# Performance work log

Hardware: AMD Instinct MI355X
Metric: run time of the kernel (lower is better)

Reference implementation:

```python
import jax, jax.numpy as jnp
import numpy as np

D_STATE = 16
LOW_RANK = 6


def _scan_fwd(t):
    # 'interwave' scan: (B, stream, signal, C, H, W) -> (stream, B, C, H*W*signal)
    st, B, C = t.shape[1], t.shape[0], t.shape[3]
    t = jnp.transpose(t, (1, 0, 3, 4, 5, 2))  # stream,B,C,H,W,signal
    return t.reshape(st, B, C, -1)


def _scan_bwd(t, sg, H, W):
    # inverse 'interwave': (stream, B, C, H*W*sg) -> (B, stream, sg, C, H, W)
    st, B, C, _ = t.shape
    t = t.reshape(st, B, C, H, W, sg)
    return jnp.transpose(t, (1, 0, 5, 2, 3, 4))


def _layernorm(t, w, b):
    # LayerNorm over last (channel) axis, eps=1e-5 (torch default)
    mu = t.mean(-1, keepdims=True)
    var = t.var(-1, keepdims=True)
    return (t - mu) * jax.lax.rsqrt(var + 1e-5) * w + b


def reference(x, x_proj_weight, dt_projs_weight, dt_projs_bias, A_logs, Ds, norm_weight, norm_bias):
    B, S, C, H, W = x.shape
    stream = S + 1
    G = 4 * stream            # scan_direction * stream groups
    N = D_STATE
    R = LOW_RANK
    L = S * H * W             # unistream_length
    i = jnp.arange(S - 1)
    j = jnp.arange(S)

    # ---- CommDiffSS2DScan (cross-scan) ----
    x_comm_0 = _scan_fwd(x[:, None])                                  # (1,B,C,L)
    x_comm_1 = _scan_fwd(jnp.swapaxes(x, -1, -2)[:, None])
    x_dif = x[:, :, None] - x[:, None, :]                             # (B,S,S,C,H,W)
    x_dif = x_dif.at[:, i, i].set(x_dif[:, i, S - 1])
    x_dif = x_dif.at[:, :, S - 1].set(x)
    x_diff_0 = _scan_fwd(x_dif)                                       # (S,B,C,L)
    x_diff_1 = _scan_fwd(jnp.swapaxes(x_dif, -1, -2))
    xs0 = jnp.concatenate([x_diff_0, x_comm_0], 0)                    # (stream,B,C,L)
    xs1 = jnp.concatenate([x_diff_1, x_comm_1], 0)
    xs = jnp.stack([xs0, xs1, xs0[..., ::-1], xs1[..., ::-1]], 0)     # (4,stream,B,C,L)
    xs = jnp.transpose(xs, (2, 0, 1, 3, 4))                           # (B,4,stream,C,L)

    # ---- input-dependent projections ----
    x_dbl = jnp.einsum('bkscl,kspc->bkspl', xs, x_proj_weight)        # (B,4,stream,R+2N,L)
    dts, Bs, Cs = jnp.split(x_dbl, [R, R + N], axis=3)
    dts = jnp.einsum('bksrl,kscr->bkscl', dts, dt_projs_weight)       # (B,4,stream,C,L)

    u = xs.reshape(B, G, C, L)
    delta = jax.nn.softplus(dts.reshape(B, G, C, L) + dt_projs_bias.reshape(G, C)[None, :, :, None])
    A = -jnp.exp(A_logs).reshape(G, C, N)
    Bm = Bs.reshape(B, G, N, L)
    Cm = Cs.reshape(B, G, N, L)

    # ---- selective scan along L ----
    def step(h, inp):
        u_, d_, b_, c_ = inp                                          # (B,G,C),(B,G,C),(B,G,N),(B,G,N)
        h = h * jnp.exp(d_[..., None] * A) + (d_ * u_)[..., None] * b_[:, :, None, :]
        return h, jnp.einsum('bgcn,bgn->bgc', h, c_)

    h0 = jnp.zeros((B, G, C, N), x.dtype)
    _, ys = jax.lax.scan(step, h0, (jnp.moveaxis(u, -1, 0), jnp.moveaxis(delta, -1, 0),
                                    jnp.moveaxis(Bm, -1, 0), jnp.moveaxis(Cm, -1, 0)))
    ys = jnp.moveaxis(ys, 0, -1) + Ds.reshape(G, C)[None, :, :, None] * u  # (B,G,C,L)

    # ---- CommDiffSS2DMerge (cross-merge) ----
    ys = jnp.transpose(ys.reshape(B, 4, stream, C, L), (1, 2, 0, 3, 4))   # (4,stream,B,C,L)
    ys = ys[:2] + ys[2:, ..., ::-1]                                       # (2,stream,B,C,L)
    yd = _scan_bwd(ys[0, :S], S, H, W) + jnp.swapaxes(_scan_bwd(ys[1, :S], S, W, H), -1, -2)
    y = yd[:, :, S - 1]
    yd = yd.at[:, i, S - 1].set(yd[:, i, i])
    yd = yd.at[:, j, j].set(0.0)
    y_dif_extend = yd.sum(2)
    y_com = (_scan_bwd(ys[0, S:], S, H, W) + jnp.swapaxes(_scan_bwd(ys[1, S:], S, W, H), -1, -2)).reshape(B, S, C, H, W)

    tocl = lambda t: jnp.transpose(t, (0, 1, 3, 4, 2))  # channels-last for out_norm
    return (_layernorm(tocl(y), norm_weight, norm_bias),
            _layernorm(tocl(y_com), norm_weight, norm_bias),
            _layernorm(tocl(y_dif_extend), norm_weight, norm_bias))


def setup_inputs() -> dict:
    key = jax.random.key(0)
    ks = jax.random.split(key, 6)
    B, S, C, H, W = 4, 2, 96, 32, 32
    stream = S + 1
    G = 4 * stream
    N, R = D_STATE, LOW_RANK
    P = N + N + R
    return {
        'x': jax.random.normal(ks[0], (B, S, C, H, W), jnp.float32),
        'x_proj_weight': jax.random.normal(ks[1], (4, stream, P, C), jnp.float32) * 0.1,
        'dt_projs_weight': jax.random.normal(ks[2], (4, stream, C, R), jnp.float32) * 0.1,
        'dt_projs_bias': jax.random.uniform(ks[3], (G * C,), jnp.float32) * 0.1,
        'A_logs': jax.random.uniform(ks[4], (G * C, N), jnp.float32),
        'Ds': jax.random.normal(ks[5], (G * C,), jnp.float32) * 0.1,
        'norm_weight': jnp.ones((C,), jnp.float32),
        'norm_bias': jnp.zeros((C,), jnp.float32),
    }
```

## Files before the change

### kernel.cpp

```cpp
#include <hip/hip_runtime.h>
#include <math.h>

typedef float f4 __attribute__((ext_vector_type(4)));
typedef float f2 __attribute__((ext_vector_type(2)));

#define L_LEN 2048
#define C_DIM 96
#define N_DIM 16
#define R_DIM 6
#define G_DIM 12
#define B_DIM 4
#define NCHUNK 64
#define CLEN 32
#define BGC (B_DIM * G_DIM * C_DIM)

#define SZ_DTS (B_DIM * G_DIM * L_LEN * R_DIM)
#define SZ_BC (B_DIM * G_DIM * N_DIM * L_LEN)
#define SZ_U6 (B_DIM * 6 * C_DIM * L_LEN)
#define SZ_Y (B_DIM * G_DIM * C_DIM * L_LEN)
#define SZ_H (BGC * NCHUNK * N_DIM)
#define SZ_X (B_DIM * 2 * C_DIM * 1024)
#define SZ_WPAD (G_DIM * 40 * C_DIM)

__device__ __forceinline__ float fexp2(float x) { return __builtin_amdgcn_exp2f(x); }

__global__ __launch_bounds__(256) void k0_xT(
    const float* __restrict__ x, float* __restrict__ xT)
{
    __shared__ float t[32][33];
    int img = blockIdx.x;
    const float* src = x + (size_t)img * 1024;
    float* dst = xT + (size_t)img * 1024;
    int tx = threadIdx.x & 31, ty = threadIdx.x >> 5;
#pragma unroll
    for (int r = 0; r < 32; r += 8) t[ty + r][tx] = src[(ty + r) * 32 + tx];
    __syncthreads();
#pragma unroll
    for (int r = 0; r < 32; r += 8) dst[(ty + r) * 32 + tx] = t[tx][ty + r];
}

__global__ __launch_bounds__(256) void k0b_padw(
    const float* __restrict__ xpw, float* __restrict__ wpad)
{
    int i = blockIdx.x * 256 + (int)threadIdx.x;
    if (i >= G_DIM * 40 * C_DIM) return;
    int g = i / (40 * C_DIM);
    int rem = i - g * 40 * C_DIM;
    int p = rem / C_DIM, c = rem - (rem / C_DIM) * C_DIM;
    wpad[i] = (p < 38) ? xpw[((size_t)g * 38 + p) * C_DIM + c] : 0.f;
}

__global__ __launch_bounds__(256) void k1_proj(
    const float* __restrict__ x, const float* __restrict__ xT,
    const float* __restrict__ wpad,
    float* __restrict__ dtsT, float* __restrict__ Bsw,
    float* __restrict__ Csw, float* __restrict__ u6T)
{
    __shared__ float Vsh[C_DIM * 68];
    __shared__ float Psh[40][68];

    int blk = blockIdx.x;
    int ltile = blk & 31;
    int bks = blk >> 5;
    int s = bks % 3;
    int k = (bks / 3) & 1;
    int b = bks / 6;
    int g = k * 3 + s;
    int gh = g + 6;
    int l0 = ltile * 64;
    int l0h = (31 - ltile) * 64;
    int bg = b * G_DIM + g;
    int bgh = b * G_DIM + gh;
    int tid = (int)threadIdx.x;

    const float* xb = (k ? xT : x) + (size_t)b * 2 * C_DIM * 1024;

#pragma unroll
    for (int j = 0; j < 6; ++j) {
        int e = tid + j * 256;
        int c = e >> 4;
        int llq = (e & 15) * 4;
        int pp = (l0 + llq) >> 1;
        f2 x0 = *(const f2*)(xb + (size_t)c * 1024 + pp);
        f2 x1 = *(const f2*)(xb + (size_t)(C_DIM + c) * 1024 + pp);
        f4 v;
        if (s == 2)      { v[0] = x0.x; v[1] = x1.x; v[2] = x0.y; v[3] = x1.y; }
        else if (s == 1) { v[0] = x1.x - x0.x; v[1] = x1.x; v[2] = x1.y - x0.y; v[3] = x1.y; }
        else             { v[0] = x0.x - x1.x; v[1] = x0.x; v[2] = x0.y - x1.y; v[3] = x0.y; }
        *(f4*)(Vsh + c * 68 + llq) = v;
    }
    __syncthreads();

    {
        size_t ub = ((size_t)(b * 6 + g) * L_LEN + l0) * C_DIM;
#pragma unroll
        for (int j = 0; j < 6; ++j) {
            int e = tid + j * 256;
            int lidx = e / 24;
            int c4 = (e - lidx * 24) * 4;
            f4 v = { Vsh[(c4 + 0) * 68 + lidx], Vsh[(c4 + 1) * 68 + lidx],
                     Vsh[(c4 + 2) * 68 + lidx], Vsh[(c4 + 3) * 68 + lidx] };
            *(f4*)(u6T + ub + (size_t)lidx * C_DIM + c4) = v;
        }
    }

    int ll = tid & 63;
    int P0 = __builtin_amdgcn_readfirstlane((tid >> 6) * 10);
    const float* wp = wpad + (size_t)g * 3840 + (size_t)P0 * C_DIM;
    const float* wph = wpad + (size_t)gh * 3840 + (size_t)P0 * C_DIM;

    float acc[10], acch[10];
#pragma unroll
    for (int p = 0; p < 10; ++p) { acc[p] = 0.f; acch[p] = 0.f; }

    for (int cb = 0; cb < C_DIM; cb += 8) {
        float vc[8], vch[8];
#pragma unroll
        for (int i = 0; i < 8; ++i) {
            vc[i] = Vsh[(cb + i) * 68 + ll];
            vch[i] = Vsh[(cb + i) * 68 + 63 - ll];
        }
#pragma unroll
        for (int p = 0; p < 10; ++p) {
#pragma unroll
            for (int q = 0; q < 2; ++q) {
                f4 w = *(const f4*)(wp + p * C_DIM + cb + q * 4);
                f4 wh = *(const f4*)(wph + p * C_DIM + cb + q * 4);
#pragma unroll
                for (int i = 0; i < 4; ++i) {
                    acc[p] = fmaf(w[i], vc[q * 4 + i], acc[p]);
                    acch[p] = fmaf(wh[i], vch[q * 4 + i], acch[p]);
                }
            }
        }
    }

#pragma unroll
    for (int gg = 0; gg < 2; ++gg) {
        __syncthreads();
#pragma unroll
        for (int p = 0; p < 10; ++p) Psh[P0 + p][ll] = gg ? acch[p] : acc[p];
        __syncthreads();
        int lb = gg ? l0h : l0;
        int bgx = gg ? bgh : bg;
        int q = tid & 3, lx = tid >> 2;
        f4 bv = { Psh[6 + q * 4 + 0][lx], Psh[6 + q * 4 + 1][lx],
                  Psh[6 + q * 4 + 2][lx], Psh[6 + q * 4 + 3][lx] };
        *(f4*)(Bsw + ((size_t)bgx * L_LEN + lb + lx) * N_DIM + q * 4) = bv;
        f4 cv = { Psh[22 + q * 4 + 0][lx], Psh[22 + q * 4 + 1][lx],
                  Psh[22 + q * 4 + 2][lx], Psh[22 + q * 4 + 3][lx] };
        *(f4*)(Csw + ((size_t)bgx * L_LEN + lb + lx) * N_DIM + q * 4) = cv;
        for (int e = tid; e < 64 * R_DIM; e += 256) {
            int lx2 = e / 6, r = e - (e / 6) * 6;
            dtsT[((size_t)bgx * L_LEN + lb + lx2) * R_DIM + r] = Psh[r][lx2];
        }
    }
}

__device__ __forceinline__ float softplus_f(float x)
{
    float sp = __logf(1.f + __expf(x));
    return (x > 60.f) ? x : sp;
}

__global__ __launch_bounds__(192) void k2_scanA(
    const float* __restrict__ dtsT, const float* __restrict__ Bsw,
    const float* __restrict__ u6T, const float* __restrict__ A_logs,
    const float* __restrict__ dtw, const float* __restrict__ dtb,
    float* __restrict__ hend, float* __restrict__ prodE)
{
    __shared__ f4 Bsh[256];
    __shared__ float Dsh[384];
    int blk = blockIdx.x;
    int chgrp = blk & 31;
    int bg = blk >> 5;
    int g = bg % G_DIM;
    int b = bg / G_DIM;
    int tid = (int)threadIdx.x;

    const f4* Bg = (const f4*)(Bsw + ((size_t)bg * L_LEN + chgrp * 64) * N_DIM);
    for (int i = tid; i < 256; i += 192) Bsh[i] = Bg[i];
    const float* Dg = dtsT + ((size_t)bg * L_LEN + chgrp * 64) * R_DIM;
    for (int i = tid; i < 384; i += 192) Dsh[i] = Dg[i];
    __syncthreads();

    int chl = tid / 96;
    int c = tid % 96;
    int ch = chgrp * 2 + chl;
    int bgc = bg * C_DIM + c;
    const bool rev = (g >= 6);
    int gu = rev ? (g - 6) : g;

    float a2[N_DIM];
    {
        const f4* Ap = (const f4*)(A_logs + ((size_t)g * C_DIM + c) * N_DIM);
        f4 Av[4] = { Ap[0], Ap[1], Ap[2], Ap[3] };
#pragma unroll
        for (int n = 0; n < N_DIM; ++n)
            a2[n] = -__expf(Av[n >> 2][n & 3]) * 1.44269504f;
    }
    float wdr[R_DIM];
    {
        const float* wdp = dtw + ((size_t)g * C_DIM + c) * R_DIM;
#pragma unroll
        for (int r = 0; r < R_DIM; ++r) wdr[r] = wdp[r];
    }
    float bias = dtb[g * C_DIM + c];

    const int LOFF = ch * CLEN;
    const float* up;
    int ustep;
    if (rev) { up = u6T + ((size_t)(b * 6 + gu) * L_LEN + (2047 - LOFF)) * C_DIM + c; ustep = -C_DIM; }
    else     { up = u6T + ((size_t)(b * 6 + gu) * L_LEN + LOFF) * C_DIM + c; ustep = C_DIM; }

    float h[N_DIM];
#pragma unroll
    for (int n = 0; n < N_DIM; ++n) h[n] = 0.f;
    float S = 0.f;

    float ubuf[4];
#pragma unroll
    for (int j = 0; j < 4; ++j) ubuf[j] = up[j * ustep];

    for (int jj = 0; jj < CLEN; jj += 4) {
        int nx = (jj + 4 < CLEN) ? jj + 4 : jj;
        float un[4];
#pragma unroll
        for (int j = 0; j < 4; ++j) un[j] = up[(nx + j) * ustep];
#pragma unroll
        for (int j = 0; j < 4; ++j) {
            int li = chl * CLEN + jj + j;
            float dt_ = bias;
#pragma unroll
            for (int r = 0; r < R_DIM; ++r) dt_ = fmaf(Dsh[li * R_DIM + r], wdr[r], dt_);
            float d = softplus_f(dt_);
            S += d;
            float du = d * ubuf[j];
            const f4* Bl = Bsh + (size_t)li * 4;
            f4 Bv[4] = { Bl[0], Bl[1], Bl[2], Bl[3] };
#pragma unroll
            for (int n = 0; n < N_DIM; ++n) {
                float e = fexp2(d * a2[n]);
                h[n] = fmaf(h[n], e, du * Bv[n >> 2][n & 3]);
            }
        }
#pragma unroll
        for (int j = 0; j < 4; ++j) ubuf[j] = un[j];
    }
    float* hp = hend + ((size_t)bgc * NCHUNK + ch) * N_DIM;
    float* pp = prodE + ((size_t)bgc * NCHUNK + ch) * N_DIM;
#pragma unroll
    for (int q = 0; q < 4; ++q) {
        f4 hv = { h[q * 4], h[q * 4 + 1], h[q * 4 + 2], h[q * 4 + 3] };
        f4 pv = { fexp2(a2[q * 4] * S), fexp2(a2[q * 4 + 1] * S),
                  fexp2(a2[q * 4 + 2] * S), fexp2(a2[q * 4 + 3] * S) };
        *(f4*)(hp + q * 4) = hv;
        *(f4*)(pp + q * 4) = pv;
    }
}

__global__ __launch_bounds__(256) void k2_fix(
    const float* __restrict__ hend, float* prodE_hstart)
{
    int t = blockIdx.x * 256 + (int)threadIdx.x;
    int n = t & 15;
    int bgc = t >> 4;
    float h = 0.f;
    for (int ch = 0; ch < NCHUNK; ++ch) {
        size_t idx = ((size_t)bgc * NCHUNK + ch) * N_DIM + n;
        float Pv = prodE_hstart[idx];
        float he = hend[idx];
        prodE_hstart[idx] = h;
        h = fmaf(h, Pv, he);
    }
}

__global__ __launch_bounds__(192) void k2_scanC(
    const float* __restrict__ dtsT, const float* __restrict__ Bsw,
    const float* __restrict__ Csw, const float* __restrict__ u6T,
    const float* __restrict__ A_logs, const float* __restrict__ Ds,
    const float* __restrict__ dtw, const float* __restrict__ dtb,
    const float* __restrict__ hstart, float* __restrict__ yssT)
{
    __shared__ f4 Bsh[256];
    __shared__ f4 Csh[256];
    __shared__ float Dsh[384];
    int blk = blockIdx.x;
    int chgrp = blk & 31;
    int bg = blk >> 5;
    int g = bg % G_DIM;
    int b = bg / G_DIM;
    int tid = (int)threadIdx.x;

    const f4* Bg = (const f4*)(Bsw + ((size_t)bg * L_LEN + chgrp * 64) * N_DIM);
    const f4* Cg = (const f4*)(Csw + ((size_t)bg * L_LEN + chgrp * 64) * N_DIM);
    for (int i = tid; i < 256; i += 192) { Bsh[i] = Bg[i]; Csh[i] = Cg[i]; }
    const float* Dg = dtsT + ((size_t)bg * L_LEN + chgrp * 64) * R_DIM;
    for (int i = tid; i < 384; i += 192) Dsh[i] = Dg[i];
    __syncthreads();

    int chl = tid / 96;
    int c = tid % 96;
    int ch = chgrp * 2 + chl;
    int bgc = bg * C_DIM + c;
    const bool rev = (g >= 6);
    int gu = rev ? (g - 6) : g;

    float a2[N_DIM];
    {
        const f4* Ap = (const f4*)(A_logs + ((size_t)g * C_DIM + c) * N_DIM);
        f4 Av[4] = { Ap[0], Ap[1], Ap[2], Ap[3] };
#pragma unroll
        for (int n = 0; n < N_DIM; ++n)
            a2[n] = -__expf(Av[n >> 2][n & 3]) * 1.44269504f;
    }
    float wdr[R_DIM];
    {
        const float* wdp = dtw + ((size_t)g * C_DIM + c) * R_DIM;
#pragma unroll
        for (int r = 0; r < R_DIM; ++r) wdr[r] = wdp[r];
    }
    float bias = dtb[g * C_DIM + c];
    float dsc = Ds[g * C_DIM + c];

    const int LOFF = ch * CLEN;
    const float* up;
    int ustep;
    if (rev) { up = u6T + ((size_t)(b * 6 + gu) * L_LEN + (2047 - LOFF)) * C_DIM + c; ustep = -C_DIM; }
    else     { up = u6T + ((size_t)(b * 6 + gu) * L_LEN + LOFF) * C_DIM + c; ustep = C_DIM; }
    float* yp = yssT + ((size_t)bg * L_LEN + LOFF) * C_DIM + c;

    float h[N_DIM];
    {
        const f4* Hp = (const f4*)(hstart + ((size_t)bgc * NCHUNK + ch) * N_DIM);
        f4 Hv[4] = { Hp[0], Hp[1], Hp[2], Hp[3] };
#pragma unroll
        for (int n = 0; n < N_DIM; ++n) h[n] = Hv[n >> 2][n & 3];
    }

    float ubuf[4];
#pragma unroll
    for (int j = 0; j < 4; ++j) ubuf[j] = up[j * ustep];

    for (int jj = 0; jj < CLEN; jj += 4) {
        int nx = (jj + 4 < CLEN) ? jj + 4 : jj;
        float un[4];
#pragma unroll
        for (int j = 0; j < 4; ++j) un[j] = up[(nx + j) * ustep];
#pragma unroll
        for (int j = 0; j < 4; ++j) {
            int li = chl * CLEN + jj + j;
            float dt_ = bias;
#pragma unroll
            for (int r = 0; r < R_DIM; ++r) dt_ = fmaf(Dsh[li * R_DIM + r], wdr[r], dt_);
            float d = softplus_f(dt_);
            float uu = ubuf[j];
            float du = d * uu;
            const f4* Bl = Bsh + (size_t)li * 4;
            const f4* Cl = Csh + (size_t)li * 4;
            f4 Bv[4] = { Bl[0], Bl[1], Bl[2], Bl[3] };
            f4 Cv[4] = { Cl[0], Cl[1], Cl[2], Cl[3] };
            float y0 = dsc * uu, y1 = 0.f, y2 = 0.f, y3 = 0.f;
#pragma unroll
            for (int q = 0; q < 4; ++q) {
                float e0 = fexp2(d * a2[q * 4 + 0]);
                float e1 = fexp2(d * a2[q * 4 + 1]);
                float e2 = fexp2(d * a2[q * 4 + 2]);
                float e3 = fexp2(d * a2[q * 4 + 3]);
                h[q * 4 + 0] = fmaf(h[q * 4 + 0], e0, du * Bv[q][0]);
                h[q * 4 + 1] = fmaf(h[q * 4 + 1], e1, du * Bv[q][1]);
                h[q * 4 + 2] = fmaf(h[q * 4 + 2], e2, du * Bv[q][2]);
                h[q * 4 + 3] = fmaf(h[q * 4 + 3], e3, du * Bv[q][3]);
                y0 = fmaf(h[q * 4 + 0], Cv[q][0], y0);
                y1 = fmaf(h[q * 4 + 1], Cv[q][1], y1);
                y2 = fmaf(h[q * 4 + 2], Cv[q][2], y2);
                y3 = fmaf(h[q * 4 + 3], Cv[q][3], y3);
            }
            yp[(jj + j) * C_DIM] = (y0 + y1) + (y2 + y3);
        }
#pragma unroll
        for (int j = 0; j < 4; ++j) ubuf[j] = un[j];
    }
}

__global__ __launch_bounds__(256) void k3_out(
    const float* __restrict__ yssT, const float* __restrict__ nw,
    const float* __restrict__ nb, float* __restrict__ out)
{
    __shared__ float tA[32][97];
    __shared__ float tB[32][97];
    __shared__ float ps[4][8][32];
    __shared__ float stat[4][32];

    int blk = blockIdx.x;
    int h = blk & 31;
    int bs = blk >> 5;
    int so = bs & 1;
    int b = bs >> 1;
    int tid = (int)threadIdx.x;

    auto Y = [&](int g) { return yssT + (size_t)(b * 12 + g) * L_LEN * C_DIM; };
    const float* Y0 = Y(so);
    const float* Y0r = Y(6 + so);
    const float* Y1 = Y(3 + so);
    const float* Y1r = Y(9 + so);

#pragma unroll 2
    for (int it = 0; it < 24; ++it) {
        int idx = tid + it * 256;
        int c = idx % 96, rest = idx / 96;
        int w = rest >> 1, par = rest & 1;
        int a0 = h * 64 + rest;
        int a1 = w * 64 + 2 * h + par;
        float v = Y0[(size_t)a0 * C_DIM + c] + Y0r[(size_t)(2047 - a0) * C_DIM + c]
                + Y1[(size_t)a1 * C_DIM + c] + Y1r[(size_t)(2047 - a1) * C_DIM + c];
        if (par) tA[w][c] = v; else tB[w][c] = v;
    }
    __syncthreads();

    int w = tid & 31, cg = tid >> 5;
    float sA = 0, qA = 0, sB = 0, qB = 0;
#pragma unroll
    for (int j = 0; j < 12; ++j) {
        float yv = tA[w][cg * 12 + j], dv = tB[w][cg * 12 + j];
        sA += yv; qA += yv * yv; sB += dv; qB += dv * dv;
    }
    ps[0][cg][w] = sA; ps[1][cg][w] = qA; ps[2][cg][w] = sB; ps[3][cg][w] = qB;
    __syncthreads();
    if (tid < 32) {
        int ww = tid;
        float t0 = 0, t1 = 0, t2 = 0, t3 = 0;
#pragma unroll
        for (int q = 0; q < 8; ++q) {
            t0 += ps[0][q][ww]; t1 += ps[1][q][ww];
            t2 += ps[2][q][ww]; t3 += ps[3][q][ww];
        }
        float muA = t0 * (1.f / 96.f), eqA = t1 * (1.f / 96.f);
        float muB = t2 * (1.f / 96.f), eqB = t3 * (1.f / 96.f);
        stat[0][ww] = muA; stat[1][ww] = rsqrtf(eqA - muA * muA + 1e-5f);
        stat[2][ww] = muB; stat[3][ww] = rsqrtf(eqB - muB * muB + 1e-5f);
    }
    __syncthreads();
    size_t obase = (size_t)blk * 3072;
    for (int e = tid; e < 3072; e += 256) {
        int ww = e / 96, c = e % 96;
        float wc = nw[c], bc = nb[c];
        out[obase + e] = (tA[ww][c] - stat[0][ww]) * stat[1][ww] * wc + bc;
        out[2 * 786432 + obase + e] = (tB[ww][c] - stat[2][ww]) * stat[3][ww] * wc + bc;
    }
    __syncthreads();

    const float* Y2 = Y(2);
    const float* Y2r = Y(8);
    const float* Y3 = Y(5);
    const float* Y3r = Y(11);
#pragma unroll 2
    for (int it = 0; it < 12; ++it) {
        int idx = tid + it * 256;
        int c = idx % 96, w2 = idx / 96;
        int a0 = h * 64 + 2 * w2 + so;
        int a1 = w2 * 64 + 2 * h + so;
        float v = Y2[(size_t)a0 * C_DIM + c] + Y2r[(size_t)(2047 - a0) * C_DIM + c]
                + Y3[(size_t)a1 * C_DIM + c] + Y3r[(size_t)(2047 - a1) * C_DIM + c];
        tA[w2][c] = v;
    }
    __syncthreads();
    float sC = 0, qC = 0;
#pragma unroll
    for (int j = 0; j < 12; ++j) {
        float v = tA[w][cg * 12 + j];
        sC += v; qC += v * v;
    }
    ps[0][cg][w] = sC; ps[1][cg][w] = qC;
    __syncthreads();
    if (tid < 32) {
        int ww = tid;
        float t0 = 0, t1 = 0;
#pragma unroll
        for (int q = 0; q < 8; ++q) { t0 += ps[0][q][ww]; t1 += ps[1][q][ww]; }
        float mu = t0 * (1.f / 96.f), eq = t1 * (1.f / 96.f);
        stat[0][ww] = mu; stat[1][ww] = rsqrtf(eq - mu * mu + 1e-5f);
    }
    __syncthreads();
    for (int e = tid; e < 3072; e += 256) {
        int ww = e / 96, c = e % 96;
        out[786432 + obase + e] = (tA[ww][c] - stat[0][ww]) * stat[1][ww] * nw[c] + nb[c];
    }
}

extern "C" void kernel_launch(void* const* d_in, const int* in_sizes, int n_in,
                              void* d_out, int out_size, void* d_ws, size_t ws_size,
                              hipStream_t stream)
{
    const float* x = (const float*)d_in[0];
    const float* xpw = (const float*)d_in[1];
    const float* dtw = (const float*)d_in[2];
    const float* dtb = (const float*)d_in[3];
    const float* A_logs = (const float*)d_in[4];
    const float* Ds = (const float*)d_in[5];
    const float* nw = (const float*)d_in[6];
    const float* nb = (const float*)d_in[7];
    float* out = (float*)d_out;

    float* ws = (float*)d_ws;
    float* dtsT = ws;
    float* Bsw = dtsT + SZ_DTS;
    float* Csw = Bsw + SZ_BC;
    float* u6T = Csw + SZ_BC;
    float* yssT = u6T + SZ_U6;
    float* hend = yssT + SZ_Y;
    float* prodE = hend + SZ_H;
    float* xT = prodE + SZ_H;
    float* wpad = xT + SZ_X;

    k0_xT<<<dim3(768), dim3(256), 0, stream>>>(x, xT);
    k0b_padw<<<dim3(180), dim3(256), 0, stream>>>(xpw, wpad);
    k1_proj<<<dim3(24 * 32), dim3(256), 0, stream>>>(x, xT, wpad, dtsT, Bsw, Csw, u6T);
    k2_scanA<<<dim3(48 * 32), dim3(192), 0, stream>>>(dtsT, Bsw, u6T, A_logs, dtw, dtb, hend, prodE);
    k2_fix<<<dim3(288), dim3(256), 0, stream>>>(hend, prodE);
    k2_scanC<<<dim3(48 * 32), dim3(192), 0, stream>>>(dtsT, Bsw, Csw, u6T, A_logs, Ds, dtw, dtb, prodE, yssT);
    k3_out<<<dim3(256), dim3(256), 0, stream>>>(yssT, nw, nb, out);
}
```

Before: 154.3 us.

## Scan kernels read B/C/dt directly as wave-uniform loads in single-wave blocks

The two scan kernels drop the shared-memory staging of B, C and dt rows and the block-wide barrier, and instead read them straight from global memory with addresses that are uniform across the wave, so they can become scalar loads. Blocks shrink from 192 threads to one 64-lane wave covering one chunk and half of the channels. The dt projection buffer is padded to 8 entries per position for aligned access. This wastes 32 of every 128 lanes on channel padding and relies on the scalar cache for reuse.

```diff
diff --git a/kernel.cpp b/kernel.cpp
--- a/kernel.cpp
+++ b/kernel.cpp
@@ -14,7 +14,7 @@
 #define CLEN 32
 #define BGC (B_DIM * G_DIM * C_DIM)
 
-#define SZ_DTS (B_DIM * G_DIM * L_LEN * R_DIM)
+#define SZ_DTS8 (B_DIM * G_DIM * L_LEN * 8)
 #define SZ_BC (B_DIM * G_DIM * N_DIM * L_LEN)
 #define SZ_U6 (B_DIM * 6 * C_DIM * L_LEN)
 #define SZ_Y (B_DIM * G_DIM * C_DIM * L_LEN)
@@ -53,7 +53,7 @@
 __global__ __launch_bounds__(256) void k1_proj(
     const float* __restrict__ x, const float* __restrict__ xT,
     const float* __restrict__ wpad,
-    float* __restrict__ dtsT, float* __restrict__ Bsw,
+    float* __restrict__ dts8, float* __restrict__ Bsw,
     float* __restrict__ Csw, float* __restrict__ u6T)
 {
     __shared__ float Vsh[C_DIM * 68];
@@ -150,9 +150,9 @@
         f4 cv = { Psh[22 + q * 4 + 0][lx], Psh[22 + q * 4 + 1][lx],
                   Psh[22 + q * 4 + 2][lx], Psh[22 + q * 4 + 3][lx] };
         *(f4*)(Csw + ((size_t)bgx * L_LEN + lb + lx) * N_DIM + q * 4) = cv;
-        for (int e = tid; e < 64 * R_DIM; e += 256) {
-            int lx2 = e / 6, r = e - (e / 6) * 6;
-            dtsT[((size_t)bgx * L_LEN + lb + lx2) * R_DIM + r] = Psh[r][lx2];
+        for (int e = tid; e < 64 * 8; e += 256) {
+            int lx2 = e >> 3, r = e & 7;
+            dts8[((size_t)bgx * L_LEN + lb + lx2) * 8 + r] = (r < 6) ? Psh[r][lx2] : 0.f;
         }
     }
 }
@@ -163,37 +163,32 @@
     return (x > 60.f) ? x : sp;
 }
 
-__global__ __launch_bounds__(192) void k2_scanA(
-    const float* __restrict__ dtsT, const float* __restrict__ Bsw,
+__global__ __launch_bounds__(64) void k2_scanA(
+    const float* __restrict__ dts8, const float* __restrict__ Bsw,
     const float* __restrict__ u6T, const float* __restrict__ A_logs,
     const float* __restrict__ dtw, const float* __restrict__ dtb,
     float* __restrict__ hend, float* __restrict__ prodE)
 {
-    __shared__ f4 Bsh[256];
-    __shared__ float Dsh[384];
+    int lane = (int)threadIdx.x;
     int blk = blockIdx.x;
-    int chgrp = blk & 31;
-    int bg = blk >> 5;
+    int ctile = blk & 1;
+    int ch = (blk >> 1) & 63;
+    int bg = blk >> 7;
     int g = bg % G_DIM;
     int b = bg / G_DIM;
-    int tid = (int)threadIdx.x;
-
-    const f4* Bg = (const f4*)(Bsw + ((size_t)bg * L_LEN + chgrp * 64) * N_DIM);
-    for (int i = tid; i < 256; i += 192) Bsh[i] = Bg[i];
-    const float* Dg = dtsT + ((size_t)bg * L_LEN + chgrp * 64) * R_DIM;
-    for (int i = tid; i < 384; i += 192) Dsh[i] = Dg[i];
-    __syncthreads();
-
-    int chl = tid / 96;
-    int c = tid % 96;
-    int ch = chgrp * 2 + chl;
-    int bgc = bg * C_DIM + c;
+    int c = ctile * 64 + lane;
+    const bool act = (c < C_DIM);
+    int cc = act ? c : (C_DIM - 1);
     const bool rev = (g >= 6);
     int gu = rev ? (g - 6) : g;
+    const int LOFF = ch * CLEN;
+
+    const float* Brow = Bsw + ((size_t)bg * L_LEN + LOFF) * N_DIM;
+    const float* Drow = dts8 + ((size_t)bg * L_LEN + LOFF) * 8;
 
     float a2[N_DIM];
     {
-        const f4* Ap = (const f4*)(A_logs + ((size_t)g * C_DIM + c) * N_DIM);
+        const f4* Ap = (const f4*)(A_logs + ((size_t)g * C_DIM + cc) * N_DIM);
         f4 Av[4] = { Ap[0], Ap[1], Ap[2], Ap[3] };
 #pragma unroll
         for (int n = 0; n < N_DIM; ++n)
@@ -201,61 +196,48 @@
     }
     float wdr[R_DIM];
     {
-        const float* wdp = dtw + ((size_t)g * C_DIM + c) * R_DIM;
+        const float* wdp = dtw + ((size_t)g * C_DIM + cc) * R_DIM;
 #pragma unroll
         for (int r = 0; r < R_DIM; ++r) wdr[r] = wdp[r];
     }
-    float bias = dtb[g * C_DIM + c];
-
-    const int LOFF = ch * CLEN;
+    float bias = dtb[g * C_DIM + cc];
+
     const float* up;
-    int ustep;
-    if (rev) { up = u6T + ((size_t)(b * 6 + gu) * L_LEN + (2047 - LOFF)) * C_DIM + c; ustep = -C_DIM; }
-    else     { up = u6T + ((size_t)(b * 6 + gu) * L_LEN + LOFF) * C_DIM + c; ustep = C_DIM; }
+    int us;
+    if (rev) { up = u6T + ((size_t)(b * 6 + gu) * L_LEN + (2047 - LOFF)) * C_DIM + cc; us = -C_DIM; }
+    else     { up = u6T + ((size_t)(b * 6 + gu) * L_LEN + LOFF) * C_DIM + cc; us = C_DIM; }
 
     float h[N_DIM];
 #pragma unroll
     for (int n = 0; n < N_DIM; ++n) h[n] = 0.f;
     float S = 0.f;
 
-    float ubuf[4];
-#pragma unroll
-    for (int j = 0; j < 4; ++j) ubuf[j] = up[j * ustep];
-
-    for (int jj = 0; jj < CLEN; jj += 4) {
-        int nx = (jj + 4 < CLEN) ? jj + 4 : jj;
-        float un[4];
-#pragma unroll
-        for (int j = 0; j < 4; ++j) un[j] = up[(nx + j) * ustep];
-#pragma unroll
-        for (int j = 0; j < 4; ++j) {
-            int li = chl * CLEN + jj + j;
-            float dt_ = bias;
-#pragma unroll
-            for (int r = 0; r < R_DIM; ++r) dt_ = fmaf(Dsh[li * R_DIM + r], wdr[r], dt_);
-            float d = softplus_f(dt_);
-            S += d;
-            float du = d * ubuf[j];
-            const f4* Bl = Bsh + (size_t)li * 4;
-            f4 Bv[4] = { Bl[0], Bl[1], Bl[2], Bl[3] };
-#pragma unroll
-            for (int n = 0; n < N_DIM; ++n) {
-                float e = fexp2(d * a2[n]);
-                h[n] = fmaf(h[n], e, du * Bv[n >> 2][n & 3]);
-            }
-        }
-#pragma unroll
-        for (int j = 0; j < 4; ++j) ubuf[j] = un[j];
-    }
-    float* hp = hend + ((size_t)bgc * NCHUNK + ch) * N_DIM;
-    float* pp = prodE + ((size_t)bgc * NCHUNK + ch) * N_DIM;
-#pragma unroll
-    for (int q = 0; q < 4; ++q) {
-        f4 hv = { h[q * 4], h[q * 4 + 1], h[q * 4 + 2], h[q * 4 + 3] };
-        f4 pv = { fexp2(a2[q * 4] * S), fexp2(a2[q * 4 + 1] * S),
-                  fexp2(a2[q * 4 + 2] * S), fexp2(a2[q * 4 + 3] * S) };
-        *(f4*)(hp + q * 4) = hv;
-        *(f4*)(pp + q * 4) = pv;
+#pragma unroll 2
+    for (int j = 0; j < CLEN; ++j) {
+        float dt_ = bias;
+#pragma unroll
+        for (int r = 0; r < R_DIM; ++r) dt_ = fmaf(Drow[j * 8 + r], wdr[r], dt_);
+        float d = softplus_f(dt_);
+        S += d;
+        float du = d * up[j * us];
+#pragma unroll
+        for (int n = 0; n < N_DIM; ++n) {
+            float e = fexp2(d * a2[n]);
+            h[n] = fmaf(h[n], e, du * Brow[j * N_DIM + n]);
+        }
+    }
+    if (act) {
+        int bgc = bg * C_DIM + c;
+        float* hp = hend + ((size_t)bgc * NCHUNK + ch) * N_DIM;
+        float* pp = prodE + ((size_t)bgc * NCHUNK + ch) * N_DIM;
+#pragma unroll
+        for (int q = 0; q < 4; ++q) {
+            f4 hv = { h[q * 4], h[q * 4 + 1], h[q * 4 + 2], h[q * 4 + 3] };
+            f4 pv = { fexp2(a2[q * 4] * S), fexp2(a2[q * 4 + 1] * S),
+                      fexp2(a2[q * 4 + 2] * S), fexp2(a2[q * 4 + 3] * S) };
+            *(f4*)(hp + q * 4) = hv;
+            *(f4*)(pp + q * 4) = pv;
+        }
     }
 }
 
@@ -275,40 +257,34 @@
     }
 }
 
-__global__ __launch_bounds__(192) void k2_scanC(
-    const float* __restrict__ dtsT, const float* __restrict__ Bsw,
+__global__ __launch_bounds__(64) void k2_scanC(
+    const float* __restrict__ dts8, const float* __restrict__ Bsw,
     const float* __restrict__ Csw, const float* __restrict__ u6T,
     const float* __restrict__ A_logs, const float* __restrict__ Ds,
     const float* __restrict__ dtw, const float* __restrict__ dtb,
     const float* __restrict__ hstart, float* __restrict__ yssT)
 {
-    __shared__ f4 Bsh[256];
-    __shared__ f4 Csh[256];
-    __shared__ float Dsh[384];
+    int lane = (int)threadIdx.x;
     int blk = blockIdx.x;
-    int chgrp = blk & 31;
-    int bg = blk >> 5;
+    int ctile = blk & 1;
+    int ch = (blk >> 1) & 63;
+    int bg = blk >> 7;
     int g = bg % G_DIM;
     int b = bg / G_DIM;
-    int tid = (int)threadIdx.x;
-
-    const f4* Bg = (const f4*)(Bsw + ((size_t)bg * L_LEN + chgrp * 64) * N_DIM);
-    const f4* Cg = (const f4*)(Csw + ((size_t)bg * L_LEN + chgrp * 64) * N_DIM);
-    for (int i = tid; i < 256; i += 192) { Bsh[i] = Bg[i]; Csh[i] = Cg[i]; }
-    const float* Dg = dtsT + ((size_t)bg * L_LEN + chgrp * 64) * R_DIM;
-    for (int i = tid; i < 384; i += 192) Dsh[i] = Dg[i];
-    __syncthreads();
-
-    int chl = tid / 96;
-    int c = tid % 96;
-    int ch = chgrp * 2 + chl;
-    int bgc = bg * C_DIM + c;
+    int c = ctile * 64 + lane;
+    const bool act = (c < C_DIM);
+    int cc = act ? c : (C_DIM - 1);
     const bool rev = (g >= 6);
     int gu = rev ? (g - 6) : g;
+    const int LOFF = ch * CLEN;
+
+    const float* Brow = Bsw + ((size_t)bg * L_LEN + LOFF) * N_DIM;
+    const float* Crow = Csw + ((size_t)bg * L_LEN + LOFF) * N_DIM;
+    const float* Drow = dts8 + ((size_t)bg * L_LEN + LOFF) * 8;
 
     float a2[N_DIM];
     {
-        const f4* Ap = (const f4*)(A_logs + ((size_t)g * C_DIM + c) * N_DIM);
+        const f4* Ap = (const f4*)(A_logs + ((size_t)g * C_DIM + cc) * N_DIM);
         f4 Av[4] = { Ap[0], Ap[1], Ap[2], Ap[3] };
 #pragma unroll
         for (int n = 0; n < N_DIM; ++n)
@@ -316,70 +292,53 @@
     }
     float wdr[R_DIM];
     {
-        const float* wdp = dtw + ((size_t)g * C_DIM + c) * R_DIM;
+        const float* wdp = dtw + ((size_t)g * C_DIM + cc) * R_DIM;
 #pragma unroll
         for (int r = 0; r < R_DIM; ++r) wdr[r] = wdp[r];
     }
-    float bias = dtb[g * C_DIM + c];
-    float dsc = Ds[g * C_DIM + c];
-
-    const int LOFF = ch * CLEN;
+    float bias = dtb[g * C_DIM + cc];
+    float dsc = Ds[g * C_DIM + cc];
+
     const float* up;
-    int ustep;
-    if (rev) { up = u6T + ((size_t)(b * 6 + gu) * L_LEN + (2047 - LOFF)) * C_DIM + c; ustep = -C_DIM; }
-    else     { up = u6T + ((size_t)(b * 6 + gu) * L_LEN + LOFF) * C_DIM + c; ustep = C_DIM; }
+    int us;
+    if (rev) { up = u6T + ((size_t)(b * 6 + gu) * L_LEN + (2047 - LOFF)) * C_DIM + cc; us = -C_DIM; }
+    else     { up = u6T + ((size_t)(b * 6 + gu) * L_LEN + LOFF) * C_DIM + cc; us = C_DIM; }
     float* yp = yssT + ((size_t)bg * L_LEN + LOFF) * C_DIM + c;
 
     float h[N_DIM];
     {
+        int bgc = bg * C_DIM + cc;
         const f4* Hp = (const f4*)(hstart + ((size_t)bgc * NCHUNK + ch) * N_DIM);
         f4 Hv[4] = { Hp[0], Hp[1], Hp[2], Hp[3] };
 #pragma unroll
         for (int n = 0; n < N_DIM; ++n) h[n] = Hv[n >> 2][n & 3];
     }
 
-    float ubuf[4];
-#pragma unroll
-    for (int j = 0; j < 4; ++j) ubuf[j] = up[j * ustep];
-
-    for (int jj = 0; jj < CLEN; jj += 4) {
-        int nx = (jj + 4 < CLEN) ? jj + 4 : jj;
-        float un[4];
-#pragma unroll
-        for (int j = 0; j < 4; ++j) un[j] = up[(nx + j) * ustep];
-#pragma unroll
-        for (int j = 0; j < 4; ++j) {
-            int li = chl * CLEN + jj + j;
-            float dt_ = bias;
-#pragma unroll
-            for (int r = 0; r < R_DIM; ++r) dt_ = fmaf(Dsh[li * R_DIM + r], wdr[r], dt_);
-            float d = softplus_f(dt_);
-            float uu = ubuf[j];
-            float du = d * uu;
-            const f4* Bl = Bsh + (size_t)li * 4;
-            const f4* Cl = Csh + (size_t)li * 4;
-            f4 Bv[4] = { Bl[0], Bl[1], Bl[2], Bl[3] };
-            f4 Cv[4] = { Cl[0], Cl[1], Cl[2], Cl[3] };
-            float y0 = dsc * uu, y1 = 0.f, y2 = 0.f, y3 = 0.f;
-#pragma unroll
-            for (int q = 0; q < 4; ++q) {
-                float e0 = fexp2(d * a2[q * 4 + 0]);
-                float e1 = fexp2(d * a2[q * 4 + 1]);
-                float e2 = fexp2(d * a2[q * 4 + 2]);
-                float e3 = fexp2(d * a2[q * 4 + 3]);
-                h[q * 4 + 0] = fmaf(h[q * 4 + 0], e0, du * Bv[q][0]);
-                h[q * 4 + 1] = fmaf(h[q * 4 + 1], e1, du * Bv[q][1]);
-                h[q * 4 + 2] = fmaf(h[q * 4 + 2], e2, du * Bv[q][2]);
-                h[q * 4 + 3] = fmaf(h[q * 4 + 3], e3, du * Bv[q][3]);
-                y0 = fmaf(h[q * 4 + 0], Cv[q][0], y0);
-                y1 = fmaf(h[q * 4 + 1], Cv[q][1], y1);
-                y2 = fmaf(h[q * 4 + 2], Cv[q][2], y2);
-                y3 = fmaf(h[q * 4 + 3], Cv[q][3], y3);
-            }
-            yp[(jj + j) * C_DIM] = (y0 + y1) + (y2 + y3);
-        }
-#pragma unroll
-        for (int j = 0; j < 4; ++j) ubuf[j] = un[j];
+#pragma unroll 2
+    for (int j = 0; j < CLEN; ++j) {
+        float dt_ = bias;
+#pragma unroll
+        for (int r = 0; r < R_DIM; ++r) dt_ = fmaf(Drow[j * 8 + r], wdr[r], dt_);
+        float d = softplus_f(dt_);
+        float uu = up[j * us];
+        float du = d * uu;
+        float y0 = dsc * uu, y1 = 0.f, y2 = 0.f, y3 = 0.f;
+#pragma unroll
+        for (int q = 0; q < 4; ++q) {
+            float e0 = fexp2(d * a2[q * 4 + 0]);
+            float e1 = fexp2(d * a2[q * 4 + 1]);
+            float e2 = fexp2(d * a2[q * 4 + 2]);
+            float e3 = fexp2(d * a2[q * 4 + 3]);
+            h[q * 4 + 0] = fmaf(h[q * 4 + 0], e0, du * Brow[j * N_DIM + q * 4 + 0]);
+            h[q * 4 + 1] = fmaf(h[q * 4 + 1], e1, du * Brow[j * N_DIM + q * 4 + 1]);
+            h[q * 4 + 2] = fmaf(h[q * 4 + 2], e2, du * Brow[j * N_DIM + q * 4 + 2]);
+            h[q * 4 + 3] = fmaf(h[q * 4 + 3], e3, du * Brow[j * N_DIM + q * 4 + 3]);
+            y0 = fmaf(h[q * 4 + 0], Crow[j * N_DIM + q * 4 + 0], y0);
+            y1 = fmaf(h[q * 4 + 1], Crow[j * N_DIM + q * 4 + 1], y1);
+            y2 = fmaf(h[q * 4 + 2], Crow[j * N_DIM + q * 4 + 2], y2);
+            y3 = fmaf(h[q * 4 + 3], Crow[j * N_DIM + q * 4 + 3], y3);
+        }
+        if (act) yp[j * C_DIM] = (y0 + y1) + (y2 + y3);
     }
 }
 
@@ -503,8 +462,8 @@
     float* out = (float*)d_out;
 
     float* ws = (float*)d_ws;
-    float* dtsT = ws;
-    float* Bsw = dtsT + SZ_DTS;
+    float* dts8 = ws;
+    float* Bsw = dts8 + SZ_DTS8;
     float* Csw = Bsw + SZ_BC;
     float* u6T = Csw + SZ_BC;
     float* yssT = u6T + SZ_U6;
@@ -515,9 +474,9 @@
 
     k0_xT<<<dim3(768), dim3(256), 0, stream>>>(x, xT);
     k0b_padw<<<dim3(180), dim3(256), 0, stream>>>(xpw, wpad);
-    k1_proj<<<dim3(24 * 32), dim3(256), 0, stream>>>(x, xT, wpad, dtsT, Bsw, Csw, u6T);
-    k2_scanA<<<dim3(48 * 32), dim3(192), 0, stream>>>(dtsT, Bsw, u6T, A_logs, dtw, dtb, hend, prodE);
+    k1_proj<<<dim3(24 * 32), dim3(256), 0, stream>>>(x, xT, wpad, dts8, Bsw, Csw, u6T);
+    k2_scanA<<<dim3(48 * 128), dim3(64), 0, stream>>>(dts8, Bsw, u6T, A_logs, dtw, dtb, hend, prodE);
     k2_fix<<<dim3(288), dim3(256), 0, stream>>>(hend, prodE);
-    k2_scanC<<<dim3(48 * 32), dim3(192), 0, stream>>>(dtsT, Bsw, Csw, u6T, A_logs, Ds, dtw, dtb, prodE, yssT);
+    k2_scanC<<<dim3(48 * 128), dim3(64), 0, stream>>>(dts8, Bsw, Csw, u6T, A_logs, Ds, dtw, dtb, prodE, yssT);
     k3_out<<<dim3(256), dim3(256), 0, stream>>>(yssT, nw, nb, out);
 }
```

After: 179.5 us. 1.16x slower.

## Precompute softplus delta in projection kernel and store chunk delta sums

Applied to the files above, without the earlier changes.

The dt low-rank projection and softplus move into the projection kernel, which now writes a full per-channel delta tensor. The two scan passes read delta directly instead of each recomputing the rank-6 dot product and softplus per element. The first scan pass stores only the per-chunk delta sum, and the fix kernel computes the chunk decay products itself. The workspace is also reshuffled so xT and the padded weights alias the y buffer. This trades transcendental work in the scans for much more memory traffic, since delta is written and read at B*G*L*C size, 16x the old dts buffer.

```diff
diff --git a/kernel.cpp b/kernel.cpp
--- a/kernel.cpp
+++ b/kernel.cpp
@@ -14,15 +14,22 @@
 #define CLEN 32
 #define BGC (B_DIM * G_DIM * C_DIM)
 
-#define SZ_DTS (B_DIM * G_DIM * L_LEN * R_DIM)
+#define SZ_DELTA (B_DIM * G_DIM * L_LEN * C_DIM)
 #define SZ_BC (B_DIM * G_DIM * N_DIM * L_LEN)
 #define SZ_U6 (B_DIM * 6 * C_DIM * L_LEN)
 #define SZ_Y (B_DIM * G_DIM * C_DIM * L_LEN)
 #define SZ_H (BGC * NCHUNK * N_DIM)
+#define SZ_S (BGC * NCHUNK)
 #define SZ_X (B_DIM * 2 * C_DIM * 1024)
 #define SZ_WPAD (G_DIM * 40 * C_DIM)
 
 __device__ __forceinline__ float fexp2(float x) { return __builtin_amdgcn_exp2f(x); }
+
+__device__ __forceinline__ float softplus_f(float x)
+{
+    float sp = __logf(1.f + __expf(x));
+    return (x > 20.f) ? x : sp;
+}
 
 __global__ __launch_bounds__(256) void k0_xT(
     const float* __restrict__ x, float* __restrict__ xT)
@@ -52,8 +59,9 @@
 
 __global__ __launch_bounds__(256) void k1_proj(
     const float* __restrict__ x, const float* __restrict__ xT,
-    const float* __restrict__ wpad,
-    float* __restrict__ dtsT, float* __restrict__ Bsw,
+    const float* __restrict__ wpad, const float* __restrict__ dtw,
+    const float* __restrict__ dtb,
+    float* __restrict__ deltaT, float* __restrict__ Bsw,
     float* __restrict__ Csw, float* __restrict__ u6T)
 {
     __shared__ float Vsh[C_DIM * 68];
@@ -143,6 +151,7 @@
         __syncthreads();
         int lb = gg ? l0h : l0;
         int bgx = gg ? bgh : bg;
+        int gx = gg ? gh : g;
         int q = tid & 3, lx = tid >> 2;
         f4 bv = { Psh[6 + q * 4 + 0][lx], Psh[6 + q * 4 + 1][lx],
                   Psh[6 + q * 4 + 2][lx], Psh[6 + q * 4 + 3][lx] };
@@ -150,27 +159,26 @@
         f4 cv = { Psh[22 + q * 4 + 0][lx], Psh[22 + q * 4 + 1][lx],
                   Psh[22 + q * 4 + 2][lx], Psh[22 + q * 4 + 3][lx] };
         *(f4*)(Csw + ((size_t)bgx * L_LEN + lb + lx) * N_DIM + q * 4) = cv;
-        for (int e = tid; e < 64 * R_DIM; e += 256) {
-            int lx2 = e / 6, r = e - (e / 6) * 6;
-            dtsT[((size_t)bgx * L_LEN + lb + lx2) * R_DIM + r] = Psh[r][lx2];
-        }
-    }
-}
-
-__device__ __forceinline__ float softplus_f(float x)
-{
-    float sp = __logf(1.f + __expf(x));
-    return (x > 60.f) ? x : sp;
+
+        const float* wdg = dtw + (size_t)gx * C_DIM * R_DIM;
+        const float* biasg = dtb + gx * C_DIM;
+        size_t db = ((size_t)bgx * L_LEN + lb) * C_DIM;
+        for (int e = tid; e < 64 * C_DIM; e += 256) {
+            int lidx = e / 96, c = e - (e / 96) * 96;
+            float dsum = biasg[c];
+#pragma unroll
+            for (int r = 0; r < R_DIM; ++r) dsum = fmaf(Psh[r][lidx], wdg[c * R_DIM + r], dsum);
+            deltaT[db + (size_t)lidx * C_DIM + c] = softplus_f(dsum);
+        }
+    }
 }
 
 __global__ __launch_bounds__(192) void k2_scanA(
-    const float* __restrict__ dtsT, const float* __restrict__ Bsw,
+    const float* __restrict__ deltaT, const float* __restrict__ Bsw,
     const float* __restrict__ u6T, const float* __restrict__ A_logs,
-    const float* __restrict__ dtw, const float* __restrict__ dtb,
-    float* __restrict__ hend, float* __restrict__ prodE)
+    float* __restrict__ hend, float* __restrict__ Sbuf)
 {
     __shared__ f4 Bsh[256];
-    __shared__ float Dsh[384];
     int blk = blockIdx.x;
     int chgrp = blk & 31;
     int bg = blk >> 5;
@@ -180,8 +188,6 @@
 
     const f4* Bg = (const f4*)(Bsw + ((size_t)bg * L_LEN + chgrp * 64) * N_DIM);
     for (int i = tid; i < 256; i += 192) Bsh[i] = Bg[i];
-    const float* Dg = dtsT + ((size_t)bg * L_LEN + chgrp * 64) * R_DIM;
-    for (int i = tid; i < 384; i += 192) Dsh[i] = Dg[i];
     __syncthreads();
 
     int chl = tid / 96;
@@ -199,41 +205,32 @@
         for (int n = 0; n < N_DIM; ++n)
             a2[n] = -__expf(Av[n >> 2][n & 3]) * 1.44269504f;
     }
-    float wdr[R_DIM];
-    {
-        const float* wdp = dtw + ((size_t)g * C_DIM + c) * R_DIM;
-#pragma unroll
-        for (int r = 0; r < R_DIM; ++r) wdr[r] = wdp[r];
-    }
-    float bias = dtb[g * C_DIM + c];
 
     const int LOFF = ch * CLEN;
+    const float* dp = deltaT + ((size_t)bg * L_LEN + LOFF) * C_DIM + c;
     const float* up;
-    int ustep;
-    if (rev) { up = u6T + ((size_t)(b * 6 + gu) * L_LEN + (2047 - LOFF)) * C_DIM + c; ustep = -C_DIM; }
-    else     { up = u6T + ((size_t)(b * 6 + gu) * L_LEN + LOFF) * C_DIM + c; ustep = C_DIM; }
+    int us;
+    if (rev) { up = u6T + ((size_t)(b * 6 + gu) * L_LEN + (2047 - LOFF)) * C_DIM + c; us = -C_DIM; }
+    else     { up = u6T + ((size_t)(b * 6 + gu) * L_LEN + LOFF) * C_DIM + c; us = C_DIM; }
 
     float h[N_DIM];
 #pragma unroll
     for (int n = 0; n < N_DIM; ++n) h[n] = 0.f;
     float S = 0.f;
 
-    float ubuf[4];
-#pragma unroll
-    for (int j = 0; j < 4; ++j) ubuf[j] = up[j * ustep];
+    float dbuf[4], ubuf[4];
+#pragma unroll
+    for (int j = 0; j < 4; ++j) { dbuf[j] = dp[j * C_DIM]; ubuf[j] = up[j * us]; }
 
     for (int jj = 0; jj < CLEN; jj += 4) {
         int nx = (jj + 4 < CLEN) ? jj + 4 : jj;
-        float un[4];
-#pragma unroll
-        for (int j = 0; j < 4; ++j) un[j] = up[(nx + j) * ustep];
+        float dn[4], un[4];
+#pragma unroll
+        for (int j = 0; j < 4; ++j) { dn[j] = dp[(nx + j) * C_DIM]; un[j] = up[(nx + j) * us]; }
 #pragma unroll
         for (int j = 0; j < 4; ++j) {
             int li = chl * CLEN + jj + j;
-            float dt_ = bias;
-#pragma unroll
-            for (int r = 0; r < R_DIM; ++r) dt_ = fmaf(Dsh[li * R_DIM + r], wdr[r], dt_);
-            float d = softplus_f(dt_);
+            float d = dbuf[j];
             S += d;
             float du = d * ubuf[j];
             const f4* Bl = Bsh + (size_t)li * 4;
@@ -245,46 +242,45 @@
             }
         }
 #pragma unroll
-        for (int j = 0; j < 4; ++j) ubuf[j] = un[j];
+        for (int j = 0; j < 4; ++j) { dbuf[j] = dn[j]; ubuf[j] = un[j]; }
     }
     float* hp = hend + ((size_t)bgc * NCHUNK + ch) * N_DIM;
-    float* pp = prodE + ((size_t)bgc * NCHUNK + ch) * N_DIM;
 #pragma unroll
     for (int q = 0; q < 4; ++q) {
         f4 hv = { h[q * 4], h[q * 4 + 1], h[q * 4 + 2], h[q * 4 + 3] };
-        f4 pv = { fexp2(a2[q * 4] * S), fexp2(a2[q * 4 + 1] * S),
-                  fexp2(a2[q * 4 + 2] * S), fexp2(a2[q * 4 + 3] * S) };
         *(f4*)(hp + q * 4) = hv;
-        *(f4*)(pp + q * 4) = pv;
-    }
+    }
+    Sbuf[(size_t)bgc * NCHUNK + ch] = S;
 }
 
 __global__ __launch_bounds__(256) void k2_fix(
-    const float* __restrict__ hend, float* prodE_hstart)
+    const float* __restrict__ Sbuf, const float* __restrict__ A_logs, float* hh)
 {
     int t = blockIdx.x * 256 + (int)threadIdx.x;
     int n = t & 15;
     int bgc = t >> 4;
+    int c = bgc % C_DIM;
+    int g = (bgc / C_DIM) % G_DIM;
+    float a2 = -__expf(A_logs[((size_t)g * C_DIM + c) * N_DIM + n]) * 1.44269504f;
+    const float* Sp = Sbuf + (size_t)bgc * NCHUNK;
     float h = 0.f;
     for (int ch = 0; ch < NCHUNK; ++ch) {
         size_t idx = ((size_t)bgc * NCHUNK + ch) * N_DIM + n;
-        float Pv = prodE_hstart[idx];
-        float he = hend[idx];
-        prodE_hstart[idx] = h;
-        h = fmaf(h, Pv, he);
+        float he = hh[idx];
+        float P = fexp2(a2 * Sp[ch]);
+        hh[idx] = h;
+        h = fmaf(h, P, he);
     }
 }
 
 __global__ __launch_bounds__(192) void k2_scanC(
-    const float* __restrict__ dtsT, const float* __restrict__ Bsw,
+    const float* __restrict__ deltaT, const float* __restrict__ Bsw,
     const float* __restrict__ Csw, const float* __restrict__ u6T,
     const float* __restrict__ A_logs, const float* __restrict__ Ds,
-    const float* __restrict__ dtw, const float* __restrict__ dtb,
     const float* __restrict__ hstart, float* __restrict__ yssT)
 {
     __shared__ f4 Bsh[256];
     __shared__ f4 Csh[256];
-    __shared__ float Dsh[384];
     int blk = blockIdx.x;
     int chgrp = blk & 31;
     int bg = blk >> 5;
@@ -295,8 +291,6 @@
     const f4* Bg = (const f4*)(Bsw + ((size_t)bg * L_LEN + chgrp * 64) * N_DIM);
     const f4* Cg = (const f4*)(Csw + ((size_t)bg * L_LEN + chgrp * 64) * N_DIM);
     for (int i = tid; i < 256; i += 192) { Bsh[i] = Bg[i]; Csh[i] = Cg[i]; }
-    const float* Dg = dtsT + ((size_t)bg * L_LEN + chgrp * 64) * R_DIM;
-    for (int i = tid; i < 384; i += 192) Dsh[i] = Dg[i];
     __syncthreads();
 
     int chl = tid / 96;
@@ -314,20 +308,14 @@
         for (int n = 0; n < N_DIM; ++n)
             a2[n] = -__expf(Av[n >> 2][n & 3]) * 1.44269504f;
     }
-    float wdr[R_DIM];
-    {
-        const float* wdp = dtw + ((size_t)g * C_DIM + c) * R_DIM;
-#pragma unroll
-        for (int r = 0; r < R_DIM; ++r) wdr[r] = wdp[r];
-    }
-    float bias = dtb[g * C_DIM + c];
     float dsc = Ds[g * C_DIM + c];
 
     const int LOFF = ch * CLEN;
+    const float* dp = deltaT + ((size_t)bg * L_LEN + LOFF) * C_DIM + c;
     const float* up;
-    int ustep;
-    if (rev) { up = u6T + ((size_t)(b * 6 + gu) * L_LEN + (2047 - LOFF)) * C_DIM + c; ustep = -C_DIM; }
-    else     { up = u6T + ((size_t)(b * 6 + gu) * L_LEN + LOFF) * C_DIM + c; ustep = C_DIM; }
+    int us;
+    if (rev) { up = u6T + ((size_t)(b * 6 + gu) * L_LEN + (2047 - LOFF)) * C_DIM + c; us = -C_DIM; }
+    else     { up = u6T + ((size_t)(b * 6 + gu) * L_LEN + LOFF) * C_DIM + c; us = C_DIM; }
     float* yp = yssT + ((size_t)bg * L_LEN + LOFF) * C_DIM + c;
 
     float h[N_DIM];
@@ -338,22 +326,19 @@
         for (int n = 0; n < N_DIM; ++n) h[n] = Hv[n >> 2][n & 3];
     }
 
-    float ubuf[4];
-#pragma unroll
-    for (int j = 0; j < 4; ++j) ubuf[j] = up[j * ustep];
+    float dbuf[4], ubuf[4];
+#pragma unroll
+    for (int j = 0; j < 4; ++j) { dbuf[j] = dp[j * C_DIM]; ubuf[j] = up[j * us]; }
 
     for (int jj = 0; jj < CLEN; jj += 4) {
         int nx = (jj + 4 < CLEN) ? jj + 4 : jj;
-        float un[4];
-#pragma unroll
-        for (int j = 0; j < 4; ++j) un[j] = up[(nx + j) * ustep];
+        float dn[4], un[4];
+#pragma unroll
+        for (int j = 0; j < 4; ++j) { dn[j] = dp[(nx + j) * C_DIM]; un[j] = up[(nx + j) * us]; }
 #pragma unroll
         for (int j = 0; j < 4; ++j) {
             int li = chl * CLEN + jj + j;
-            float dt_ = bias;
-#pragma unroll
-            for (int r = 0; r < R_DIM; ++r) dt_ = fmaf(Dsh[li * R_DIM + r], wdr[r], dt_);
-            float d = softplus_f(dt_);
+            float d = dbuf[j];
             float uu = ubuf[j];
             float du = d * uu;
             const f4* Bl = Bsh + (size_t)li * 4;
@@ -379,7 +364,7 @@
             yp[(jj + j) * C_DIM] = (y0 + y1) + (y2 + y3);
         }
 #pragma unroll
-        for (int j = 0; j < 4; ++j) ubuf[j] = un[j];
+        for (int j = 0; j < 4; ++j) { dbuf[j] = dn[j]; ubuf[j] = un[j]; }
     }
 }
 
@@ -503,21 +488,21 @@
     float* out = (float*)d_out;
 
     float* ws = (float*)d_ws;
-    float* dtsT = ws;
-    float* Bsw = dtsT + SZ_DTS;
+    float* deltaT = ws;
+    float* Bsw = deltaT + SZ_DELTA;
     float* Csw = Bsw + SZ_BC;
     float* u6T = Csw + SZ_BC;
     float* yssT = u6T + SZ_U6;
+    float* xT = yssT;
+    float* wpad = yssT + SZ_X;
     float* hend = yssT + SZ_Y;
-    float* prodE = hend + SZ_H;
-    float* xT = prodE + SZ_H;
-    float* wpad = xT + SZ_X;
+    float* Sbuf = hend + SZ_H;
 
     k0_xT<<<dim3(768), dim3(256), 0, stream>>>(x, xT);
     k0b_padw<<<dim3(180), dim3(256), 0, stream>>>(xpw, wpad);
-    k1_proj<<<dim3(24 * 32), dim3(256), 0, stream>>>(x, xT, wpad, dtsT, Bsw, Csw, u6T);
-    k2_scanA<<<dim3(48 * 32), dim3(192), 0, stream>>>(dtsT, Bsw, u6T, A_logs, dtw, dtb, hend, prodE);
-    k2_fix<<<dim3(288), dim3(256), 0, stream>>>(hend, prodE);
-    k2_scanC<<<dim3(48 * 32), dim3(192), 0, stream>>>(dtsT, Bsw, Csw, u6T, A_logs, Ds, dtw, dtb, prodE, yssT);
+    k1_proj<<<dim3(24 * 32), dim3(256), 0, stream>>>(x, xT, wpad, dtw, dtb, deltaT, Bsw, Csw, u6T);
+    k2_scanA<<<dim3(48 * 32), dim3(192), 0, stream>>>(deltaT, Bsw, u6T, A_logs, hend, Sbuf);
+    k2_fix<<<dim3(288), dim3(256), 0, stream>>>(Sbuf, A_logs, hend);
+    k2_scanC<<<dim3(48 * 32), dim3(192), 0, stream>>>(deltaT, Bsw, Csw, u6T, A_logs, Ds, hend, yssT);
     k3_out<<<dim3(256), dim3(256), 0, stream>>>(yssT, nw, nb, out);
 }
```

After: 150.1 us. 2.7% less time.
